# Performance work log

Measured on AMD Instinct MI355X. Metric: run time of the kernel, lower is better.

The kernel has to match this reference:

```python
import jax, jax.numpy as jnp
import numpy as np

LN_EPS = 1e-12


def _layernorm(x, gamma, beta):
    mu = jnp.mean(x, axis=-1, keepdims=True)
    var = jnp.var(x, axis=-1, keepdims=True)
    return gamma * (x - mu) / jnp.sqrt(var + LN_EPS) + beta


def setup_inputs() -> dict:
    key = jax.random.key(0)
    ks = jax.random.split(key, 8)
    B, N, C, H = 8, 8192, 512, 8
    FFN = 4 * C
    s_attn = 1.0 / np.sqrt(C)
    s_ffn1 = 1.0 / np.sqrt(C)
    s_ffn2 = 1.0 / np.sqrt(FFN)
    return {
        "x": jax.random.normal(ks[0], (B, N, C), jnp.float32),
        "wq": jax.random.normal(ks[1], (C, C), jnp.float32) * s_attn,
        "bq": jnp.zeros((C,), jnp.float32),
        "wk": jax.random.normal(ks[2], (C, C), jnp.float32) * s_attn,
        "bk": jnp.zeros((C,), jnp.float32),
        "wv": jax.random.normal(ks[3], (C, C), jnp.float32) * s_attn,
        "bv": jnp.zeros((C,), jnp.float32),
        "wo": jax.random.normal(ks[4], (C, C), jnp.float32) * s_attn,
        "bo": jnp.zeros((C,), jnp.float32),
        "gamma1": jnp.ones((C,), jnp.float32),
        "beta1": jnp.zeros((C,), jnp.float32),
        "w_fc1": jax.random.normal(ks[5], (C, FFN), jnp.float32) * s_ffn1,
        "b_fc1": jnp.zeros((FFN,), jnp.float32),
        "w_fc2": jax.random.normal(ks[6], (FFN, C), jnp.float32) * s_ffn2,
        "b_fc2": jnp.zeros((C,), jnp.float32),
        "gamma2": jnp.ones((C,), jnp.float32),
        "beta2": jnp.zeros((C,), jnp.float32),
        "window_size": 64,
        "n_head": 8,
    }


def reference(x, wq, bq, wk, bk, wv, bv, wo, bo, gamma1, beta1,
              w_fc1, b_fc1, w_fc2, b_fc2, gamma2, beta2,
              window_size, n_head):
    B, N, C = x.shape
    ws = window_size
    H = n_head
    dh = C // H

    # window partition: [B, N, C] -> [B*N/ws, ws, C]
    xw = x.reshape(B * N // ws, ws, C)
    shortcut = xw

    # windowed multi-head self-attention
    q = (xw @ wq + bq).reshape(-1, ws, H, dh)
    k = (xw @ wk + bk).reshape(-1, ws, H, dh)
    v = (xw @ wv + bv).reshape(-1, ws, H, dh)
    scale = 1.0 / jnp.sqrt(jnp.asarray(dh, xw.dtype))
    attn = jnp.einsum('wqhd,wkhd->whqk', q, k) * scale  # [nw, H, ws, ws]
    attn = jax.nn.softmax(attn, axis=-1)
    out = jnp.einsum('whqk,wkhd->wqhd', attn, v).reshape(-1, ws, C)
    out = out @ wo + bo

    # residual + LN1
    h = _layernorm(out + shortcut, gamma1, beta1)

    # MLP (fc1 -> GELU -> fc2), residual + LN2
    ff = jax.nn.gelu(h @ w_fc1 + b_fc1, approximate=False) @ w_fc2 + b_fc2
    h = _layernorm(ff + h, gamma2, beta2)

    # window reverse: -> [B, N, C]
    return h.reshape(B, N, C)
```

## Files before the change

kernel.cpp:

```cpp
#include <hip/hip_runtime.h>

typedef __attribute__((ext_vector_type(8))) short bf16x8;
typedef __attribute__((ext_vector_type(4))) float f32x4;

__device__ __forceinline__ short f2b(float f) {
  unsigned u = __builtin_bit_cast(unsigned, f);
  unsigned r = (u + 0x7FFFu + ((u >> 16) & 1u)) >> 16;
  return (short)r;
}
__device__ __forceinline__ float b2f(short s) {
  unsigned u = ((unsigned)(unsigned short)s) << 16;
  return __builtin_bit_cast(float, u);
}

__device__ __forceinline__ void gload16(const void* g, void* l) {
  __builtin_amdgcn_global_load_lds(
      (const __attribute__((address_space(1))) void*)g,
      (__attribute__((address_space(3))) void*)l, 16, 0, 0);
}

__device__ __forceinline__ float gelu_f(float v) {
  float u = v * (0.7978845608f + 0.0356774081f * v * v);
  float a = fabsf(u);
  float e = __expf(-2.f * a);
  float t = (1.f - e) * __builtin_amdgcn_rcpf(1.f + e);
  t = (u < 0.f) ? -t : t;
  return 0.5f * v * (1.f + t);
}

__global__ void cvt_bf16_vec(const float* __restrict__ src, short* __restrict__ dst, long n) {
  long i = ((long)blockIdx.x * 256 + threadIdx.x) * 8;
  if (i >= n) return;
  f32x4 a = *(const f32x4*)(src + i);
  f32x4 b = *(const f32x4*)(src + i + 4);
  bf16x8 o;
#pragma unroll
  for (int j = 0; j < 4; j++) o[j] = f2b(a[j]);
#pragma unroll
  for (int j = 0; j < 4; j++) o[j + 4] = f2b(b[j]);
  *(bf16x8*)(dst + i) = o;
}

__global__ void transpose_cvt_t(const float* __restrict__ src, short* __restrict__ dst,
                                int K, int N) {
  __shared__ float tile[32][33];
  const int n0 = blockIdx.x * 32, k0 = blockIdx.y * 32;
  const int j = threadIdx.x & 31, i0 = threadIdx.x >> 5;
#pragma unroll
  for (int r = 0; r < 4; r++) {
    int i = i0 + r * 8;
    tile[i][j] = src[(long)(k0 + i) * N + n0 + j];
  }
  __syncthreads();
#pragma unroll
  for (int r = 0; r < 4; r++) {
    int i = i0 + r * 8;
    dst[(long)(n0 + i) * K + k0 + j] = f2b(tile[j][i]);
  }
}

__global__ void pack_bias3(const float* __restrict__ b0, const float* __restrict__ b1,
                           const float* __restrict__ b2, float* __restrict__ out) {
  int t = blockIdx.x * 256 + threadIdx.x;
  if (t >= 1536) return;
  out[t] = (t < 512) ? b0[t] : ((t < 1024) ? b1[t - 512] : b2[t - 1024]);
}

template <int EPI>
__global__ __launch_bounds__(256, 4) void gemm_bt(
    const short* __restrict__ A, const short* __restrict__ Bt,
    const float* __restrict__ bias, const float* __restrict__ resF,
    const short* __restrict__ resB, void* __restrict__ Cout, int K, int ldc, int gxN) {
  __shared__ short As[128 * 32];
  __shared__ short Bs[128 * 32];
  const int t = threadIdx.x;
  const int w = t >> 6, lane = t & 63;
  const int lr = lane & 15, lg = lane >> 4;

  const int nwg = gridDim.x;
  const int orig = blockIdx.x;
  const int q = nwg >> 3, r = nwg & 7, xcd = orig & 7, idx = orig >> 3;
  const int swz = (xcd < r ? xcd * (q + 1) : r * (q + 1) + (xcd - r) * q) + idx;
  const long m0 = (long)(swz / gxN) * 128;
  const int n0 = (swz % gxN) * 128;

  const int wm = (w >> 1) * 64, wn = (w & 1) * 64;

  f32x4 acc[4][4];
#pragma unroll
  for (int i = 0; i < 4; i++)
#pragma unroll
    for (int j = 0; j < 4; j++) acc[i][j] = f32x4{0.f, 0.f, 0.f, 0.f};

  const int r0 = t >> 2;
  const int kc0 = (t & 3) * 8;
  const short* Ag = A + m0 * K + (long)r0 * K + kc0;
  const short* Bg = Bt + n0 * (long)K + (long)r0 * K + kc0;

  for (int kt = 0; kt < K; kt += 32) {
    gload16(Ag + kt, As + t * 8);
    gload16(Ag + (long)64 * K + kt, As + t * 8 + 2048);
    gload16(Bg + kt, Bs + t * 8);
    gload16(Bg + (long)64 * K + kt, Bs + t * 8 + 2048);
    __syncthreads();
    bf16x8 a[4], b[4];
#pragma unroll
    for (int mi = 0; mi < 4; mi++)
      a[mi] = *(const bf16x8*)(As + (wm + mi * 16 + lr) * 32 + lg * 8);
#pragma unroll
    for (int nj = 0; nj < 4; nj++)
      b[nj] = *(const bf16x8*)(Bs + (wn + nj * 16 + lr) * 32 + lg * 8);
#pragma unroll
    for (int mi = 0; mi < 4; mi++)
#pragma unroll
      for (int nj = 0; nj < 4; nj++)
        acc[mi][nj] =
            __builtin_amdgcn_mfma_f32_16x16x32_bf16(a[mi], b[nj], acc[mi][nj], 0, 0, 0);
    __syncthreads();
  }

  float bv[4];
#pragma unroll
  for (int nj = 0; nj < 4; nj++) bv[nj] = bias[n0 + wn + nj * 16 + lr];

#pragma unroll
  for (int mi = 0; mi < 4; mi++)
#pragma unroll
    for (int i = 0; i < 4; i++) {
      const long row = m0 + wm + mi * 16 + lg * 4 + i;
      const long rb = row * ldc + n0 + wn + lr;
      if (EPI == 0) {
        short* p = (short*)Cout + rb;
#pragma unroll
        for (int nj = 0; nj < 4; nj++) p[nj * 16] = f2b(acc[mi][nj][i] + bv[nj]);
      } else if (EPI == 1) {
        short* p = (short*)Cout + rb;
#pragma unroll
        for (int nj = 0; nj < 4; nj++) p[nj * 16] = f2b(gelu_f(acc[mi][nj][i] + bv[nj]));
      } else if (EPI == 2) {
        float* p = (float*)Cout + rb;
        const float* rp = resF + rb;
#pragma unroll
        for (int nj = 0; nj < 4; nj++) p[nj * 16] = acc[mi][nj][i] + bv[nj] + rp[nj * 16];
      } else {
        float* p = (float*)Cout + rb;
        const short* rp = resB + rb;
#pragma unroll
        for (int nj = 0; nj < 4; nj++)
          p[nj * 16] = acc[mi][nj][i] + bv[nj] + b2f(rp[nj * 16]);
      }
    }
}

__global__ __launch_bounds__(256, 2) void attn_win(const short* __restrict__ QKV,
                                                   short* __restrict__ AO) {
  __shared__ short Vs[64 * 72];
  __shared__ short Ps[64 * 72];
  const int t = threadIdx.x, w = t >> 6, lane = t & 63;
  const int lr = lane & 15, lg = lane >> 4;
  const long base = (long)blockIdx.x * 64 * 1536;
  const long obase = (long)blockIdx.x * 64 * 512;

  for (int h = 0; h < 8; h++) {
    const int co = h * 64;
#pragma unroll
    for (int it = 0; it < 2; it++) {
      int c = t + it * 256;
      int j = c >> 3, d0 = (c & 7) * 8;
      *(bf16x8*)(Vs + j * 72 + d0) =
          *(const bf16x8*)(QKV + base + (long)j * 1536 + 1024 + co + d0);
    }
    __syncthreads();

    bf16x8 qf[2], kf[4][2];
#pragma unroll
    for (int kb = 0; kb < 2; kb++)
      qf[kb] = *(const bf16x8*)(QKV + base + (long)(w * 16 + lr) * 1536 + co + kb * 32 + lg * 8);
#pragma unroll
    for (int nj = 0; nj < 4; nj++)
#pragma unroll
      for (int kb = 0; kb < 2; kb++)
        kf[nj][kb] = *(const bf16x8*)(QKV + base + (long)(nj * 16 + lr) * 1536 + 512 + co +
                                      kb * 32 + lg * 8);

    f32x4 s[4];
#pragma unroll
    for (int nj = 0; nj < 4; nj++) {
      s[nj] = f32x4{0.f, 0.f, 0.f, 0.f};
      s[nj] = __builtin_amdgcn_mfma_f32_16x16x32_bf16(qf[0], kf[nj][0], s[nj], 0, 0, 0);
      s[nj] = __builtin_amdgcn_mfma_f32_16x16x32_bf16(qf[1], kf[nj][1], s[nj], 0, 0, 0);
      s[nj] = s[nj] * 0.125f;
    }

#pragma unroll
    for (int i = 0; i < 4; i++) {
      float mx = fmaxf(fmaxf(s[0][i], s[1][i]), fmaxf(s[2][i], s[3][i]));
#pragma unroll
      for (int off = 1; off < 16; off <<= 1) mx = fmaxf(mx, __shfl_xor(mx, off, 64));
      float sum = 0.f;
#pragma unroll
      for (int nj = 0; nj < 4; nj++) {
        float p = __expf(s[nj][i] - mx);
        s[nj][i] = p;
        sum += p;
      }
#pragma unroll
      for (int off = 1; off < 16; off <<= 1) sum += __shfl_xor(sum, off, 64);
      float inv = 1.f / sum;
#pragma unroll
      for (int nj = 0; nj < 4; nj++) s[nj][i] *= inv;
    }

#pragma unroll
    for (int nj = 0; nj < 4; nj++)
#pragma unroll
      for (int i = 0; i < 4; i++)
        Ps[(w * 16 + lg * 4 + i) * 72 + nj * 16 + lr] = f2b(s[nj][i]);

    bf16x8 pa[2];
#pragma unroll
    for (int kb = 0; kb < 2; kb++)
      pa[kb] = *(const bf16x8*)(Ps + (w * 16 + lr) * 72 + kb * 32 + lg * 8);

    f32x4 o[4];
#pragma unroll
    for (int nb = 0; nb < 4; nb++) o[nb] = f32x4{0.f, 0.f, 0.f, 0.f};
#pragma unroll
    for (int kb = 0; kb < 2; kb++)
#pragma unroll
      for (int nb = 0; nb < 4; nb++) {
        bf16x8 vb;
#pragma unroll
        for (int jj = 0; jj < 8; jj++)
          vb[jj] = Vs[(kb * 32 + lg * 8 + jj) * 72 + nb * 16 + lr];
        o[nb] = __builtin_amdgcn_mfma_f32_16x16x32_bf16(pa[kb], vb, o[nb], 0, 0, 0);
      }

#pragma unroll
    for (int nb = 0; nb < 4; nb++)
#pragma unroll
      for (int i = 0; i < 4; i++)
        AO[obase + (long)(w * 16 + lg * 4 + i) * 512 + co + nb * 16 + lr] = f2b(o[nb][i]);
    __syncthreads();
  }
}

template <int OUTB>
__global__ __launch_bounds__(256, 4) void ln_rows(const float* __restrict__ Y,
                                                  const float* __restrict__ gamma,
                                                  const float* __restrict__ beta,
                                                  short* __restrict__ Hb,
                                                  float* __restrict__ Of) {
  const int w = threadIdx.x >> 6, lane = threadIdx.x & 63;
  const long row = (long)blockIdx.x * 4 + w;
  const float* y = Y + row * 512 + lane * 8;
  f32x4 a = *(const f32x4*)(y);
  f32x4 b = *(const f32x4*)(y + 4);
  float s = a[0] + a[1] + a[2] + a[3] + b[0] + b[1] + b[2] + b[3];
  float s2 = a[0] * a[0] + a[1] * a[1] + a[2] * a[2] + a[3] * a[3] + b[0] * b[0] +
             b[1] * b[1] + b[2] * b[2] + b[3] * b[3];
#pragma unroll
  for (int off = 1; off < 64; off <<= 1) {
    s += __shfl_xor(s, off, 64);
    s2 += __shfl_xor(s2, off, 64);
  }
  float mu = s * (1.f / 512.f);
  float var = s2 * (1.f / 512.f) - mu * mu;
  float rstd = rsqrtf(fmaxf(var, 0.f) + 1e-12f);
  const int c0 = lane * 8;
  f32x4 ga = *(const f32x4*)(gamma + c0), gb = *(const f32x4*)(gamma + c0 + 4);
  f32x4 ba = *(const f32x4*)(beta + c0), bb = *(const f32x4*)(beta + c0 + 4);
  if (OUTB) {
    bf16x8 o;
#pragma unroll
    for (int j = 0; j < 4; j++) o[j] = f2b(ga[j] * ((a[j] - mu) * rstd) + ba[j]);
#pragma unroll
    for (int j = 0; j < 4; j++) o[j + 4] = f2b(gb[j] * ((b[j] - mu) * rstd) + bb[j]);
    *(bf16x8*)(Hb + row * 512 + c0) = o;
  } else {
    f32x4 o0, o1;
#pragma unroll
    for (int j = 0; j < 4; j++) o0[j] = ga[j] * ((a[j] - mu) * rstd) + ba[j];
#pragma unroll
    for (int j = 0; j < 4; j++) o1[j] = gb[j] * ((b[j] - mu) * rstd) + bb[j];
    *(f32x4*)(Of + row * 512 + c0) = o0;
    *(f32x4*)(Of + row * 512 + c0 + 4) = o1;
  }
}

extern "C" void kernel_launch(void* const* d_in, const int* in_sizes, int n_in,
                              void* d_out, int out_size, void* d_ws, size_t ws_size,
                              hipStream_t stream) {
  (void)in_sizes; (void)n_in; (void)out_size;
  const float* x = (const float*)d_in[0];
  const float* wq = (const float*)d_in[1];
  const float* bq = (const float*)d_in[2];
  const float* wk = (const float*)d_in[3];
  const float* bk = (const float*)d_in[4];
  const float* wv = (const float*)d_in[5];
  const float* bv = (const float*)d_in[6];
  const float* wo = (const float*)d_in[7];
  const float* bo = (const float*)d_in[8];
  const float* g1 = (const float*)d_in[9];
  const float* be1 = (const float*)d_in[10];
  const float* wfc1 = (const float*)d_in[11];
  const float* bfc1 = (const float*)d_in[12];
  const float* wfc2 = (const float*)d_in[13];
  const float* bfc2 = (const float*)d_in[14];
  const float* g2 = (const float*)d_in[15];
  const float* be2 = (const float*)d_in[16];

  const long T = 65536;
  char* ws = (char*)d_ws;

  short* WQKVT = (short*)(ws);
  short* WOT = WQKVT + 1536 * 512;
  short* WFC1T = WOT + 512 * 512;
  short* WFC2T = WFC1T + 2048 * 512;
  float* BQKV = (float*)(WFC2T + 512 * 2048);
  size_t woff = ((size_t)((char*)(BQKV + 1536) - ws) + 255) & ~(size_t)255;

  size_t avail = (ws_size > woff) ? (ws_size - woff) : 0;
  long Tc = T;
  while (Tc > 128 && (size_t)Tc * 7168 > avail) Tc >>= 1;
  const long nch = T / Tc;

  char* R0 = ws + woff;
  char* R1 = R0 + (size_t)Tc * 4096;
  char* R2 = R1 + (size_t)Tc * 2048;

  short* QKV = (short*)R0;
  float* Y1 = (float*)R0;
  short* FF1 = (short*)R0;
  short* XB = (short*)R1;
  short* AO = (short*)R1;
  float* Y2 = (float*)R1;
  short* H = (short*)R2;

  transpose_cvt_t<<<dim3(16, 16), 256, 0, stream>>>(wq, WQKVT, 512, 512);
  transpose_cvt_t<<<dim3(16, 16), 256, 0, stream>>>(wk, WQKVT + 512 * 512, 512, 512);
  transpose_cvt_t<<<dim3(16, 16), 256, 0, stream>>>(wv, WQKVT + 1024 * 512, 512, 512);
  transpose_cvt_t<<<dim3(16, 16), 256, 0, stream>>>(wo, WOT, 512, 512);
  transpose_cvt_t<<<dim3(64, 16), 256, 0, stream>>>(wfc1, WFC1T, 512, 2048);
  transpose_cvt_t<<<dim3(16, 64), 256, 0, stream>>>(wfc2, WFC2T, 2048, 512);
  pack_bias3<<<6, 256, 0, stream>>>(bq, bk, bv, BQKV);

  for (long c = 0; c < nch; c++) {
    const long t0 = c * Tc;
    const int mb = (int)(Tc / 128);
    cvt_bf16_vec<<<(int)(Tc / 4), 256, 0, stream>>>(x + t0 * 512, XB, Tc * 512);
    gemm_bt<0><<<mb * 12, 256, 0, stream>>>(XB, WQKVT, BQKV, nullptr, nullptr,
                                            (void*)QKV, 512, 1536, 12);
    attn_win<<<(int)(Tc / 64), 256, 0, stream>>>(QKV, AO);
    gemm_bt<2><<<mb * 4, 256, 0, stream>>>(AO, WOT, bo, x + t0 * 512, nullptr,
                                           (void*)Y1, 512, 512, 4);
    ln_rows<1><<<(int)(Tc / 4), 256, 0, stream>>>(Y1, g1, be1, H, nullptr);
    gemm_bt<1><<<mb * 16, 256, 0, stream>>>(H, WFC1T, bfc1, nullptr, nullptr,
                                            (void*)FF1, 512, 2048, 16);
    gemm_bt<3><<<mb * 4, 256, 0, stream>>>(FF1, WFC2T, bfc2, nullptr, H, (void*)Y2,
                                           2048, 512, 4);
    ln_rows<0><<<(int)(Tc / 4), 256, 0, stream>>>(Y2, g2, be2, nullptr,
                                                  (float*)d_out + t0 * 512);
  }
}
```

Measured before the change: 829.6 us.

## Triple-buffer LDS tiles in bf16 GEMM to overlap global loads with MFMA

Replaces the single-buffered LDS load/compute loop in the GEMM kernel with a three-stage ring buffer. Global-to-LDS loads are issued two K-steps ahead and guarded by vmcnt waits, and each iteration uses one barrier instead of two. The aim is to hide global memory latency behind the MFMA work. In exchange, LDS use per block triples to 48KB and launch bounds drop from 4 to 3 blocks per SM, which lowers occupancy.

```diff
diff --git a/kernel.cpp b/kernel.cpp
--- a/kernel.cpp
+++ b/kernel.cpp
@@ -67,12 +67,11 @@
 }
 
 template <int EPI>
-__global__ __launch_bounds__(256, 4) void gemm_bt(
+__global__ __launch_bounds__(256, 3) void gemm_bt(
     const short* __restrict__ A, const short* __restrict__ Bt,
     const float* __restrict__ bias, const float* __restrict__ resF,
     const short* __restrict__ resB, void* __restrict__ Cout, int K, int ldc, int gxN) {
-  __shared__ short As[128 * 32];
-  __shared__ short Bs[128 * 32];
+  __shared__ short lds[3 * 8192];
   const int t = threadIdx.x;
   const int w = t >> 6, lane = t & 63;
   const int lr = lane & 15, lg = lane >> 4;
@@ -94,30 +93,67 @@
 
   const int r0 = t >> 2;
   const int kc0 = (t & 3) * 8;
-  const short* Ag = A + m0 * K + (long)r0 * K + kc0;
-  const short* Bg = Bt + n0 * (long)K + (long)r0 * K + kc0;
-
-  for (int kt = 0; kt < K; kt += 32) {
-    gload16(Ag + kt, As + t * 8);
-    gload16(Ag + (long)64 * K + kt, As + t * 8 + 2048);
-    gload16(Bg + kt, Bs + t * 8);
-    gload16(Bg + (long)64 * K + kt, Bs + t * 8 + 2048);
-    __syncthreads();
+  const short* Ag = A + (m0 + r0) * (long)K + kc0;
+  const short* Bg = Bt + ((long)n0 + r0) * K + kc0;
+  const long half = (long)64 * K;
+
+#define STAGE(b, kt)                                   \
+  {                                                    \
+    short* d = lds + (b) * 8192 + t * 8;               \
+    gload16(Ag + (long)(kt) * 32, d);                  \
+    gload16(Ag + half + (long)(kt) * 32, d + 2048);    \
+    gload16(Bg + (long)(kt) * 32, d + 4096);           \
+    gload16(Bg + half + (long)(kt) * 32, d + 6144);    \
+  }
+
+  const int NKT = K >> 5;
+  STAGE(0, 0)
+  STAGE(1, 1)
+
+  const int aoff = (wm + lr) * 32 + lg * 8;
+  const int boff = 4096 + (wn + lr) * 32 + lg * 8;
+
+  int cb = 0, sb = 2;
+  for (int kt = 0; kt < NKT - 1; ++kt) {
+    asm volatile("s_waitcnt vmcnt(4)" ::: "memory");
+    __builtin_amdgcn_sched_barrier(0);
+    __builtin_amdgcn_s_barrier();
+    __builtin_amdgcn_sched_barrier(0);
+    if (kt + 2 < NKT) STAGE(sb, kt + 2)
+    const short* Lb = lds + cb * 8192;
     bf16x8 a[4], b[4];
 #pragma unroll
-    for (int mi = 0; mi < 4; mi++)
-      a[mi] = *(const bf16x8*)(As + (wm + mi * 16 + lr) * 32 + lg * 8);
-#pragma unroll
-    for (int nj = 0; nj < 4; nj++)
-      b[nj] = *(const bf16x8*)(Bs + (wn + nj * 16 + lr) * 32 + lg * 8);
+    for (int mi = 0; mi < 4; mi++) a[mi] = *(const bf16x8*)(Lb + aoff + mi * 512);
+#pragma unroll
+    for (int nj = 0; nj < 4; nj++) b[nj] = *(const bf16x8*)(Lb + boff + nj * 512);
 #pragma unroll
     for (int mi = 0; mi < 4; mi++)
 #pragma unroll
       for (int nj = 0; nj < 4; nj++)
         acc[mi][nj] =
             __builtin_amdgcn_mfma_f32_16x16x32_bf16(a[mi], b[nj], acc[mi][nj], 0, 0, 0);
-    __syncthreads();
-  }
+    cb = (cb == 2) ? 0 : cb + 1;
+    sb = (sb == 2) ? 0 : sb + 1;
+  }
+  {
+    asm volatile("s_waitcnt vmcnt(0)" ::: "memory");
+    __builtin_amdgcn_sched_barrier(0);
+    __builtin_amdgcn_s_barrier();
+    __builtin_amdgcn_sched_barrier(0);
+    const short* Lb = lds + cb * 8192;
+    bf16x8 a[4], b[4];
+#pragma unroll
+    for (int mi = 0; mi < 4; mi++) a[mi] = *(const bf16x8*)(Lb + aoff + mi * 512);
+#pragma unroll
+    for (int nj = 0; nj < 4; nj++) b[nj] = *(const bf16x8*)(Lb + boff + nj * 512);
+#pragma unroll
+    for (int mi = 0; mi < 4; mi++)
+#pragma unroll
+      for (int nj = 0; nj < 4; nj++)
+        acc[mi][nj] =
+            __builtin_amdgcn_mfma_f32_16x16x32_bf16(a[mi], b[nj], acc[mi][nj], 0, 0, 0);
+  }
+#undef STAGE
 
   float bv[4];
 #pragma unroll
```

Result: no change. 825.6 us (-0.5%).

## Multi-stage LDS pipeline with XOR swizzle in bf16 GEMM mainloop

Applied to the files above, without the earlier changes.

Replaces the single-buffered load/sync/compute GEMM loop with a 5-buffer ring of LDS tiles, prefetching 4 K-tiles ahead with direct global-to-LDS loads and vmcnt-based waits, using one barrier per iteration. It also XOR-swizzles the 16-byte chunk placement to reduce LDS bank conflicts and raises MFMA priority with setprio. The larger LDS footprint (80KB) drops the launch bound to 2 blocks per CU, trading occupancy for latency hiding.

```diff
diff --git a/kernel.cpp b/kernel.cpp
--- a/kernel.cpp
+++ b/kernel.cpp
@@ -67,12 +67,11 @@
 }
 
 template <int EPI>
-__global__ __launch_bounds__(256, 4) void gemm_bt(
+__global__ __launch_bounds__(256, 2) void gemm_bt(
     const short* __restrict__ A, const short* __restrict__ Bt,
     const float* __restrict__ bias, const float* __restrict__ resF,
     const short* __restrict__ resB, void* __restrict__ Cout, int K, int ldc, int gxN) {
-  __shared__ short As[128 * 32];
-  __shared__ short Bs[128 * 32];
+  __shared__ short lds[5 * 8192];
   const int t = threadIdx.x;
   const int w = t >> 6, lane = t & 63;
   const int lr = lane & 15, lg = lane >> 4;
@@ -92,32 +91,65 @@
 #pragma unroll
     for (int j = 0; j < 4; j++) acc[i][j] = f32x4{0.f, 0.f, 0.f, 0.f};
 
-  const int r0 = t >> 2;
-  const int kc0 = (t & 3) * 8;
-  const short* Ag = A + m0 * K + (long)r0 * K + kc0;
-  const short* Bg = Bt + n0 * (long)K + (long)r0 * K + kc0;
-
-  for (int kt = 0; kt < K; kt += 32) {
-    gload16(Ag + kt, As + t * 8);
-    gload16(Ag + (long)64 * K + kt, As + t * 8 + 2048);
-    gload16(Bg + kt, Bs + t * 8);
-    gload16(Bg + (long)64 * K + kt, Bs + t * 8 + 2048);
-    __syncthreads();
-    bf16x8 a[4], b[4];
-#pragma unroll
-    for (int mi = 0; mi < 4; mi++)
-      a[mi] = *(const bf16x8*)(As + (wm + mi * 16 + lr) * 32 + lg * 8);
-#pragma unroll
-    for (int nj = 0; nj < 4; nj++)
-      b[nj] = *(const bf16x8*)(Bs + (wn + nj * 16 + lr) * 32 + lg * 8);
-#pragma unroll
-    for (int mi = 0; mi < 4; mi++)
-#pragma unroll
-      for (int nj = 0; nj < 4; nj++)
-        acc[mi][nj] =
-            __builtin_amdgcn_mfma_f32_16x16x32_bf16(a[mi], b[nj], acc[mi][nj], 0, 0, 0);
-    __syncthreads();
-  }
+  const int srow = t >> 2;
+  const int schunk = (t & 3) ^ ((t >> 2) & 3);
+  const short* Ag = A + (m0 + srow) * (long)K + schunk * 8;
+  const short* Bg = Bt + ((long)n0 + srow) * K + schunk * 8;
+  const long half = (long)64 * K;
+
+#define STAGE(b, kt)                                   \
+  {                                                    \
+    short* d = lds + (b) * 8192 + t * 8;               \
+    gload16(Ag + (long)(kt) * 32, d);                  \
+    gload16(Ag + half + (long)(kt) * 32, d + 2048);    \
+    gload16(Bg + (long)(kt) * 32, d + 4096);           \
+    gload16(Bg + half + (long)(kt) * 32, d + 6144);    \
+  }
+
+  const int xsw = (lg ^ (lr & 3)) * 8;
+  const int aoff = (wm + lr) * 32 + xsw;
+  const int boff = 4096 + (wn + lr) * 32 + xsw;
+
+#define TILE_WAIT(WN)                                        \
+  asm volatile("s_waitcnt vmcnt(" #WN ")" ::: "memory");     \
+  __builtin_amdgcn_sched_barrier(0);                         \
+  __builtin_amdgcn_s_barrier();                              \
+  __builtin_amdgcn_sched_barrier(0);
+
+#define BODY(CB)                                                               \
+  {                                                                            \
+    const short* Lb = lds + (CB) * 8192;                                       \
+    bf16x8 a[4], b[4];                                                         \
+    _Pragma("unroll") for (int mi = 0; mi < 4; mi++)                           \
+        a[mi] = *(const bf16x8*)(Lb + aoff + mi * 512);                        \
+    _Pragma("unroll") for (int nj = 0; nj < 4; nj++)                           \
+        b[nj] = *(const bf16x8*)(Lb + boff + nj * 512);                        \
+    __builtin_amdgcn_s_setprio(1);                                             \
+    _Pragma("unroll") for (int mi = 0; mi < 4; mi++)                           \
+        _Pragma("unroll") for (int nj = 0; nj < 4; nj++) acc[mi][nj] =         \
+            __builtin_amdgcn_mfma_f32_16x16x32_bf16(a[mi], b[nj], acc[mi][nj], \
+                                                    0, 0, 0);                  \
+    __builtin_amdgcn_s_setprio(0);                                             \
+  }
+
+  const int NKT = K >> 5;
+  STAGE(0, 0) STAGE(1, 1) STAGE(2, 2) STAGE(3, 3)
+
+  int cb = 0, sb = 4;
+  for (int kt = 0; kt < NKT - 4; ++kt) {
+    TILE_WAIT(12)
+    STAGE(sb, kt + 4)
+    BODY(cb)
+    cb = (cb == 4) ? 0 : cb + 1;
+    sb = (sb == 4) ? 0 : sb + 1;
+  }
+  TILE_WAIT(12) BODY(cb) cb = (cb == 4) ? 0 : cb + 1;
+  TILE_WAIT(8)  BODY(cb) cb = (cb == 4) ? 0 : cb + 1;
+  TILE_WAIT(4)  BODY(cb) cb = (cb == 4) ? 0 : cb + 1;
+  TILE_WAIT(0)  BODY(cb)
+#undef STAGE
+#undef TILE_WAIT
+#undef BODY
 
   float bv[4];
 #pragma unroll
```

Result: slower. 870.3 us (+4.9%).

## Replace 128x128 GEMM with 256x256 double-buffered swizzled-LDS GEMM kernel

Applied to the files above, without the earlier changes.

All four GEMMs move from a 128x128 tile, 256-thread kernel to a 256x256 tile, 512-thread kernel. The new kernel uses 128KB of dynamic LDS with double-buffered K=64 stages, XOR-swizzled LDS layout and staggered async global-to-LDS loads interleaved across four compute phases. It also raises MFMA wave priority around the compute blocks. This cuts global traffic per FLOP and hides load latency. In exchange occupancy drops to one block per CU and the grids get smaller: the out-projection and fc2 GEMMs launch only 512 blocks.

```diff
diff --git a/kernel.cpp b/kernel.cpp
--- a/kernel.cpp
+++ b/kernel.cpp
@@ -67,87 +67,166 @@
 }
 
 template <int EPI>
-__global__ __launch_bounds__(256, 4) void gemm_bt(
+__global__ __launch_bounds__(512, 1) void gemm256(
     const short* __restrict__ A, const short* __restrict__ Bt,
     const float* __restrict__ bias, const float* __restrict__ resF,
     const short* __restrict__ resB, void* __restrict__ Cout, int K, int ldc, int gxN) {
-  __shared__ short As[128 * 32];
-  __shared__ short Bs[128 * 32];
+  extern __shared__ short lds[];
   const int t = threadIdx.x;
-  const int w = t >> 6, lane = t & 63;
+  const int lane = t & 63, w = t >> 6;
   const int lr = lane & 15, lg = lane >> 4;
-
-  const int nwg = gridDim.x;
-  const int orig = blockIdx.x;
-  const int q = nwg >> 3, r = nwg & 7, xcd = orig & 7, idx = orig >> 3;
-  const int swz = (xcd < r ? xcd * (q + 1) : r * (q + 1) + (xcd - r) * q) + idx;
-  const long m0 = (long)(swz / gxN) * 128;
-  const int n0 = (swz % gxN) * 128;
-
-  const int wm = (w >> 1) * 64, wn = (w & 1) * 64;
-
-  f32x4 acc[4][4];
-#pragma unroll
-  for (int i = 0; i < 4; i++)
+  const int wm = w >> 2, wn = w & 3;
+
+  const int nwg = gridDim.x, orig = blockIdx.x;
+  const int q8 = nwg >> 3, r8 = nwg & 7, xcd = orig & 7, idx = orig >> 3;
+  const int swz = (xcd < r8 ? xcd * (q8 + 1) : r8 * (q8 + 1) + (xcd - r8) * q8) + idx;
+  const long m0 = (long)(swz / gxN) * 256;
+  const int n0 = (swz % gxN) * 256;
+
+  f32x4 acc[8][4];
+#pragma unroll
+  for (int i = 0; i < 8; i++)
 #pragma unroll
     for (int j = 0; j < 4; j++) acc[i][j] = f32x4{0.f, 0.f, 0.f, 0.f};
 
-  const int r0 = t >> 2;
-  const int kc0 = (t & 3) * 8;
-  const short* Ag = A + m0 * K + (long)r0 * K + kc0;
-  const short* Bg = Bt + n0 * (long)K + (long)r0 * K + kc0;
-
-  for (int kt = 0; kt < K; kt += 32) {
-    gload16(Ag + kt, As + t * 8);
-    gload16(Ag + (long)64 * K + kt, As + t * 8 + 2048);
-    gload16(Bg + kt, Bs + t * 8);
-    gload16(Bg + (long)64 * K + kt, Bs + t * 8 + 2048);
-    __syncthreads();
-    bf16x8 a[4], b[4];
-#pragma unroll
-    for (int mi = 0; mi < 4; mi++)
-      a[mi] = *(const bf16x8*)(As + (wm + mi * 16 + lr) * 32 + lg * 8);
-#pragma unroll
-    for (int nj = 0; nj < 4; nj++)
-      b[nj] = *(const bf16x8*)(Bs + (wn + nj * 16 + lr) * 32 + lg * 8);
-#pragma unroll
-    for (int mi = 0; mi < 4; mi++)
-#pragma unroll
-      for (int nj = 0; nj < 4; nj++)
-        acc[mi][nj] =
-            __builtin_amdgcn_mfma_f32_16x16x32_bf16(a[mi], b[nj], acc[mi][nj], 0, 0, 0);
-    __syncthreads();
-  }
+  const int srow = t >> 3;
+  const int sch = (t & 7) ^ (srow & 7);
+  const short* sA = A + (m0 + srow) * (long)K + sch * 8;
+  const short* sB = Bt + ((long)n0 + srow) * K + sch * 8;
+  const long r64 = (long)64 * K;
+
+#define STG_A(tt, h)                                                     \
+  {                                                                      \
+    short* d_ = lds + ((tt) & 1) * 16384 + (h) * 8192 + t * 8;           \
+    const short* s_ = sA + (h) * 2 * r64 + (long)(tt) * 64;              \
+    gload16(s_, d_);                                                     \
+    gload16(s_ + r64, d_ + 4096);                                        \
+  }
+#define STG_B(tt, h)                                                     \
+  {                                                                      \
+    short* d_ = lds + 32768 + ((tt) & 1) * 16384 + (h) * 8192 + t * 8;   \
+    const short* s_ = sB + (h) * 2 * r64 + (long)(tt) * 64;              \
+    gload16(s_, d_);                                                     \
+    gload16(s_ + r64, d_ + 4096);                                        \
+  }
+
+  const int xsw0 = (lg ^ (lr & 7)) * 8;
+  const int xsw1 = ((4 + lg) ^ (lr & 7)) * 8;
+  const int aRow0 = (wm * 128 + lr) * 64;
+  const int bRow0 = 32768 + (wn * 64 + lr) * 64;
+
+#define BAR                                  \
+  {                                          \
+    __builtin_amdgcn_sched_barrier(0);       \
+    __builtin_amdgcn_s_barrier();            \
+    __builtin_amdgcn_sched_barrier(0);       \
+  }
+
+  const int NT = K >> 6;
+  STG_A(0, 0) STG_A(0, 1) STG_B(0, 0) STG_B(0, 1) STG_B(1, 0) STG_B(1, 1)
+  asm volatile("s_waitcnt vmcnt(4)" ::: "memory");
+  BAR
+
+  bf16x8 b[4][2];
+
+#define PHASE_Q(Q, STAGE_STMT, PRE_BAR2)                                       \
+  {                                                                            \
+    bf16x8 aq[2][2];                                                           \
+    _Pragma("unroll") for (int mi = 0; mi < 2; mi++) {                         \
+      aq[mi][0] =                                                              \
+          *(const bf16x8*)(lds + aRow0 + dA + ((Q) * 32 + mi * 16) * 64 + xsw0); \
+      aq[mi][1] =                                                              \
+          *(const bf16x8*)(lds + aRow0 + dA + ((Q) * 32 + mi * 16) * 64 + xsw1); \
+    }                                                                          \
+    STAGE_STMT                                                                 \
+    BAR                                                                        \
+    __builtin_amdgcn_s_setprio(1);                                             \
+    _Pragma("unroll") for (int mi = 0; mi < 2; mi++)                           \
+        _Pragma("unroll") for (int nj = 0; nj < 4; nj++) {                     \
+      acc[(Q) * 2 + mi][nj] = __builtin_amdgcn_mfma_f32_16x16x32_bf16(         \
+          aq[mi][0], b[nj][0], acc[(Q) * 2 + mi][nj], 0, 0, 0);                \
+      acc[(Q) * 2 + mi][nj] = __builtin_amdgcn_mfma_f32_16x16x32_bf16(         \
+          aq[mi][1], b[nj][1], acc[(Q) * 2 + mi][nj], 0, 0, 0);                \
+    }                                                                          \
+    __builtin_amdgcn_s_setprio(0);                                             \
+    PRE_BAR2                                                                   \
+    BAR                                                                        \
+  }
+
+  for (int tt = 0; tt < NT; ++tt) {
+    const int dA = (tt & 1) * 16384;
+    {
+#pragma unroll
+      for (int nj = 0; nj < 4; nj++) {
+        b[nj][0] = *(const bf16x8*)(lds + bRow0 + dA + nj * 1024 + xsw0);
+        b[nj][1] = *(const bf16x8*)(lds + bRow0 + dA + nj * 1024 + xsw1);
+      }
+      bf16x8 aq[2][2];
+#pragma unroll
+      for (int mi = 0; mi < 2; mi++) {
+        aq[mi][0] = *(const bf16x8*)(lds + aRow0 + dA + (mi * 16) * 64 + xsw0);
+        aq[mi][1] = *(const bf16x8*)(lds + aRow0 + dA + (mi * 16) * 64 + xsw1);
+      }
+      if (tt + 1 < NT) STG_A(tt + 1, 0)
+      BAR
+      __builtin_amdgcn_s_setprio(1);
+#pragma unroll
+      for (int mi = 0; mi < 2; mi++)
+#pragma unroll
+        for (int nj = 0; nj < 4; nj++) {
+          acc[mi][nj] = __builtin_amdgcn_mfma_f32_16x16x32_bf16(
+              aq[mi][0], b[nj][0], acc[mi][nj], 0, 0, 0);
+          acc[mi][nj] = __builtin_amdgcn_mfma_f32_16x16x32_bf16(
+              aq[mi][1], b[nj][1], acc[mi][nj], 0, 0, 0);
+        }
+      __builtin_amdgcn_s_setprio(0);
+      BAR
+    }
+    PHASE_Q(1, { if (tt + 1 < NT) STG_A(tt + 1, 1) }, {})
+    PHASE_Q(2, { if (tt + 2 < NT) STG_B(tt + 2, 0) }, {})
+    PHASE_Q(3, { if (tt + 2 < NT) STG_B(tt + 2, 1) },
+            {
+              if (tt + 2 < NT) {
+                asm volatile("s_waitcnt vmcnt(4)" ::: "memory");
+              } else if (tt + 1 < NT) {
+                asm volatile("s_waitcnt vmcnt(0)" ::: "memory");
+              }
+            })
+  }
+#undef PHASE_Q
+#undef STG_A
+#undef STG_B
+#undef BAR
 
   float bv[4];
 #pragma unroll
-  for (int nj = 0; nj < 4; nj++) bv[nj] = bias[n0 + wn + nj * 16 + lr];
-
-#pragma unroll
-  for (int mi = 0; mi < 4; mi++)
+  for (int nj = 0; nj < 4; nj++) bv[nj] = bias[n0 + wn * 64 + nj * 16 + lr];
+
+#pragma unroll
+  for (int a = 0; a < 8; a++)
 #pragma unroll
     for (int i = 0; i < 4; i++) {
-      const long row = m0 + wm + mi * 16 + lg * 4 + i;
-      const long rb = row * ldc + n0 + wn + lr;
+      const long row = m0 + wm * 128 + a * 16 + lg * 4 + i;
+      const long rb = row * ldc + n0 + wn * 64 + lr;
       if (EPI == 0) {
         short* p = (short*)Cout + rb;
 #pragma unroll
-        for (int nj = 0; nj < 4; nj++) p[nj * 16] = f2b(acc[mi][nj][i] + bv[nj]);
+        for (int nj = 0; nj < 4; nj++) p[nj * 16] = f2b(acc[a][nj][i] + bv[nj]);
       } else if (EPI == 1) {
         short* p = (short*)Cout + rb;
 #pragma unroll
-        for (int nj = 0; nj < 4; nj++) p[nj * 16] = f2b(gelu_f(acc[mi][nj][i] + bv[nj]));
+        for (int nj = 0; nj < 4; nj++) p[nj * 16] = f2b(gelu_f(acc[a][nj][i] + bv[nj]));
       } else if (EPI == 2) {
         float* p = (float*)Cout + rb;
         const float* rp = resF + rb;
 #pragma unroll
-        for (int nj = 0; nj < 4; nj++) p[nj * 16] = acc[mi][nj][i] + bv[nj] + rp[nj * 16];
+        for (int nj = 0; nj < 4; nj++) p[nj * 16] = acc[a][nj][i] + bv[nj] + rp[nj * 16];
       } else {
         float* p = (float*)Cout + rb;
         const short* rp = resB + rb;
 #pragma unroll
         for (int nj = 0; nj < 4; nj++)
-          p[nj * 16] = acc[mi][nj][i] + bv[nj] + b2f(rp[nj * 16]);
+          p[nj * 16] = acc[a][nj][i] + bv[nj] + b2f(rp[nj * 16]);
       }
     }
 }
@@ -322,7 +401,7 @@
 
   size_t avail = (ws_size > woff) ? (ws_size - woff) : 0;
   long Tc = T;
-  while (Tc > 128 && (size_t)Tc * 7168 > avail) Tc >>= 1;
+  while (Tc > 256 && (size_t)Tc * 7168 > avail) Tc >>= 1;
   const long nch = T / Tc;
 
   char* R0 = ws + woff;
@@ -345,20 +424,21 @@
   transpose_cvt_t<<<dim3(16, 64), 256, 0, stream>>>(wfc2, WFC2T, 2048, 512);
   pack_bias3<<<6, 256, 0, stream>>>(bq, bk, bv, BQKV);
 
+  const size_t LDSB = 131072;
   for (long c = 0; c < nch; c++) {
     const long t0 = c * Tc;
-    const int mb = (int)(Tc / 128);
+    const int mb = (int)(Tc / 256);
     cvt_bf16_vec<<<(int)(Tc / 4), 256, 0, stream>>>(x + t0 * 512, XB, Tc * 512);
-    gemm_bt<0><<<mb * 12, 256, 0, stream>>>(XB, WQKVT, BQKV, nullptr, nullptr,
-                                            (void*)QKV, 512, 1536, 12);
+    gemm256<0><<<mb * 6, 512, LDSB, stream>>>(XB, WQKVT, BQKV, nullptr, nullptr,
+                                              (void*)QKV, 512, 1536, 6);
     attn_win<<<(int)(Tc / 64), 256, 0, stream>>>(QKV, AO);
-    gemm_bt<2><<<mb * 4, 256, 0, stream>>>(AO, WOT, bo, x + t0 * 512, nullptr,
-                                           (void*)Y1, 512, 512, 4);
+    gemm256<2><<<mb * 2, 512, LDSB, stream>>>(AO, WOT, bo, x + t0 * 512, nullptr,
+                                              (void*)Y1, 512, 512, 2);
     ln_rows<1><<<(int)(Tc / 4), 256, 0, stream>>>(Y1, g1, be1, H, nullptr);
-    gemm_bt<1><<<mb * 16, 256, 0, stream>>>(H, WFC1T, bfc1, nullptr, nullptr,
-                                            (void*)FF1, 512, 2048, 16);
-    gemm_bt<3><<<mb * 4, 256, 0, stream>>>(FF1, WFC2T, bfc2, nullptr, H, (void*)Y2,
-                                           2048, 512, 4);
+    gemm256<1><<<mb * 8, 512, LDSB, stream>>>(H, WFC1T, bfc1, nullptr, nullptr,
+                                              (void*)FF1, 512, 2048, 8);
+    gemm256<3><<<mb * 2, 512, LDSB, stream>>>(FF1, WFC2T, bfc2, nullptr, H, (void*)Y2,
+                                              2048, 512, 2);
     ln_rows<0><<<(int)(Tc / 4), 256, 0, stream>>>(Y2, g2, be2, nullptr,
                                                   (float*)d_out + t0 * 512);
   }
```

Result: faster. 771.5 us (-7.0%).
